# Kernel optimization log

Measured on AMD Instinct MI355X. Metric: run time of the kernel, lower is better.

## Reference

```python
import jax, jax.numpy as jnp
import numpy as np

E, D, H, N = 8, 1024, 4096, 8192  # experts, model dim, moe intermediate, total tokens


def setup_inputs() -> dict:
    key = jax.random.key(0)
    k0, k1, k2, k3 = jax.random.split(key, 4)
    x = jax.random.normal(k0, (N, D), jnp.float32)
    # PrimeRL layout: w1,w3: [E, H, D]; w2: [E, D, H]
    w1 = jax.random.normal(k1, (E, H, D), jnp.float32) * 0.02
    w2 = jax.random.normal(k2, (E, D, H), jnp.float32) * 0.02
    w3 = jax.random.normal(k3, (E, H, D), jnp.float32) * 0.02
    num_tokens_per_expert = jnp.full((E,), N // E, dtype=jnp.int32)  # balanced, sums to N
    return {"x": x, "w1": w1, "w2": w2, "w3": w3,
            "num_tokens_per_expert": num_tokens_per_expert}


def reference(x, w1, w2, w3, num_tokens_per_expert):
    # grouped MoE FFN: per expert e over its contiguous token block,
    #   h = gelu_tanh(x @ w1[e].T) * (x @ w3[e].T); out = h @ w2[e].T
    # torch path casts to bf16 for the grouped mm, casts output back.
    gs = num_tokens_per_expert.astype(jnp.int32)  # group sizes = offsets via cumsum
    xb = x.astype(jnp.bfloat16)
    w1t = jnp.swapaxes(w1, -2, -1).astype(jnp.bfloat16)  # [E, D, H]
    w2t = jnp.swapaxes(w2, -2, -1).astype(jnp.bfloat16)  # [E, H, D]
    w3t = jnp.swapaxes(w3, -2, -1).astype(jnp.bfloat16)  # [E, D, H]
    g = jax.lax.ragged_dot(xb, w1t, gs)                  # [N, H]
    h = jax.nn.gelu(g, approximate=True) * jax.lax.ragged_dot(xb, w3t, gs)
    out = jax.lax.ragged_dot(h, w2t, gs).astype(x.dtype)  # [N, D]
    return out
```

## Files before the change

kernel.cpp:

```cpp
#include <hip/hip_runtime.h>
#include <hip/hip_bf16.h>

#define E_ 8
#define D_ 1024
#define H_ 4096
#define N_ 8192

typedef __attribute__((ext_vector_type(8))) short bf16x8;
typedef __attribute__((ext_vector_type(4))) float f32x4;
typedef unsigned short u16;

static __device__ __forceinline__ u16 f2bf(float f) {
    unsigned int u = __float_as_uint(f);
    u += 0x7fffu + ((u >> 16) & 1u);
    return (u16)(u >> 16);
}

static __device__ __forceinline__ void st_bf4(u16* p, float4 v) {
    union { u16 u[4]; unsigned long long ll; } t;
    t.u[0] = f2bf(v.x); t.u[1] = f2bf(v.y); t.u[2] = f2bf(v.z); t.u[3] = f2bf(v.w);
    *(unsigned long long*)p = t.ll;
}

static __device__ __forceinline__ float gelu_tanh(float x) {
    float x3 = x * x * x;
    float z = 0.7978845608028654f * (x + 0.044715f * x3);
    float t = 1.0f - 2.0f / (1.0f + __expf(2.0f * z));
    return 0.5f * x * (1.0f + t);
}

static __device__ __forceinline__ int expert_of(const int* __restrict__ ntpe, int row) {
    int acc = 0;
    #pragma unroll
    for (int i = 0; i < E_; ++i) {
        acc += ntpe[i];
        if (row < acc) return i;
    }
    return E_ - 1;
}

#define GLD16(gp, lp) __builtin_amdgcn_global_load_lds( \
    (const __attribute__((address_space(1))) void*)(gp), \
    (__attribute__((address_space(3))) void*)(lp), 16, 0, 0)

#define CVT_XBLK 512
#define CVT_WBLK 2048
#define CVT_NBLK (CVT_XBLK + 3 * CVT_WBLK)

__global__ __launch_bounds__(256) void cvt_all2(
    const float* __restrict__ x, const float* __restrict__ w1,
    const float* __restrict__ w2, const float* __restrict__ w3,
    u16* __restrict__ xb, u16* __restrict__ w1b,
    u16* __restrict__ w2b, u16* __restrict__ w3b)
{
    int b = blockIdx.x;
    const float* src; u16* dst; int n8; int b0; int nb;
    if (b < CVT_XBLK) {
        src = x; dst = xb; n8 = N_ * D_ / 8; b0 = 0; nb = CVT_XBLK;
    } else if (b < CVT_XBLK + CVT_WBLK) {
        src = w1; dst = w1b; n8 = E_ * H_ * D_ / 8; b0 = CVT_XBLK; nb = CVT_WBLK;
    } else if (b < CVT_XBLK + 2 * CVT_WBLK) {
        src = w2; dst = w2b; n8 = E_ * D_ * H_ / 8; b0 = CVT_XBLK + CVT_WBLK; nb = CVT_WBLK;
    } else {
        src = w3; dst = w3b; n8 = E_ * H_ * D_ / 8; b0 = CVT_XBLK + 2 * CVT_WBLK; nb = CVT_WBLK;
    }
    int t = (b - b0) * 256 + threadIdx.x;
    int stride = nb * 256;
    const float4* s4 = (const float4*)src;
    for (int i = t; i < n8; i += stride) {
        float4 a = s4[i * 2];
        float4 c = s4[i * 2 + 1];
        union { u16 u[8]; bf16x8 v; } o;
        o.u[0] = f2bf(a.x); o.u[1] = f2bf(a.y); o.u[2] = f2bf(a.z); o.u[3] = f2bf(a.w);
        o.u[4] = f2bf(c.x); o.u[5] = f2bf(c.y); o.u[6] = f2bf(c.z); o.u[7] = f2bf(c.w);
        *(bf16x8*)(dst + (size_t)i * 8) = o.v;
    }
}

#define EPIT 72

__global__ __launch_bounds__(256, 3) void moe_gemm13_fast(
    const u16* __restrict__ xb, const u16* __restrict__ w1b,
    const u16* __restrict__ w3b, const int* __restrict__ ntpe,
    u16* __restrict__ hbuf)
{
    __shared__ u16 smem[128 * EPIT];
    u16* sA  = smem;
    u16* sB1 = smem + 4096;
    u16* sB2 = smem + 6144;

    const int tid = threadIdx.x;
    const int m0 = blockIdx.y * 128, n0 = blockIdx.x * 64;
    const int e = expert_of(ntpe, m0);
    const int wave = tid >> 6, lane = tid & 63;
    const int wm = (wave >> 1) * 64, wn = (wave & 1) * 32;
    const int fr = lane & 15, quad = lane >> 4;

    const u16* Ag  = xb  + (size_t)m0 * D_;
    const u16* B1g = w1b + ((size_t)e * H_ + n0) * D_;
    const u16* B2g = w3b + ((size_t)e * H_ + n0) * D_;

    const int srA = wave * 32 + (lane >> 2);
    const int srB = wave * 16 + (lane >> 2);
    const int scol = (lane & 3) * 8;

    f32x4 accg[4][2], accu[4][2];
    #pragma unroll
    for (int i = 0; i < 4; ++i)
        #pragma unroll
        for (int j = 0; j < 2; ++j) {
            accg[i][j] = (f32x4){0.f, 0.f, 0.f, 0.f};
            accu[i][j] = (f32x4){0.f, 0.f, 0.f, 0.f};
        }

    for (int k0 = 0; k0 < D_; k0 += 32) {
        #pragma unroll
        for (int c = 0; c < 2; ++c)
            GLD16(Ag + (size_t)(srA + c * 16) * D_ + k0 + scol, sA + (wave * 32 + c * 16) * 32);
        GLD16(B1g + (size_t)srB * D_ + k0 + scol, sB1 + wave * 16 * 32);
        GLD16(B2g + (size_t)srB * D_ + k0 + scol, sB2 + wave * 16 * 32);
        __syncthreads();

        bf16x8 fa[4], fb1[2], fb2[2];
        #pragma unroll
        for (int i = 0; i < 4; ++i)
            fa[i] = *(const bf16x8*)(&sA[(wm + i * 16 + fr) * 32 + quad * 8]);
        #pragma unroll
        for (int j = 0; j < 2; ++j) {
            fb1[j] = *(const bf16x8*)(&sB1[(wn + j * 16 + fr) * 32 + quad * 8]);
            fb2[j] = *(const bf16x8*)(&sB2[(wn + j * 16 + fr) * 32 + quad * 8]);
        }
        #pragma unroll
        for (int i = 0; i < 4; ++i)
            #pragma unroll
            for (int j = 0; j < 2; ++j) {
                accg[i][j] = __builtin_amdgcn_mfma_f32_16x16x32_bf16(fa[i], fb1[j], accg[i][j], 0, 0, 0);
                accu[i][j] = __builtin_amdgcn_mfma_f32_16x16x32_bf16(fa[i], fb2[j], accu[i][j], 0, 0, 0);
            }
        __syncthreads();
    }

    #pragma unroll
    for (int i = 0; i < 4; ++i) {
        int rl = wm + i * 16 + quad * 4;
        #pragma unroll
        for (int j = 0; j < 2; ++j) {
            int cl = wn + j * 16 + fr;
            #pragma unroll
            for (int r = 0; r < 4; ++r) {
                float hv = gelu_tanh(accg[i][j][r]) * accu[i][j][r];
                smem[(rl + r) * EPIT + cl] = f2bf(hv);
            }
        }
    }
    __syncthreads();
    #pragma unroll
    for (int it = 0; it < 4; ++it) {
        int chunk = it * 256 + tid;
        int row = chunk >> 3;
        int col = (chunk & 7) * 8;
        bf16x8 v = *(const bf16x8*)(&smem[row * EPIT + col]);
        *(bf16x8*)(&hbuf[(size_t)(m0 + row) * H_ + n0 + col]) = v;
    }
}

__global__ __launch_bounds__(256, 3) void moe_gemm2_fast(
    const u16* __restrict__ hbuf, const u16* __restrict__ w2b,
    const int* __restrict__ ntpe, float* __restrict__ out)
{
    __shared__ u16 sA[128 * 32], sB[128 * 32];
    const int tid = threadIdx.x;
    const int m0 = blockIdx.y * 128, n0 = blockIdx.x * 128;
    const int e = expert_of(ntpe, m0);
    const int wave = tid >> 6, lane = tid & 63;
    const int wm = (wave >> 1) * 64, wn = (wave & 1) * 64;
    const int fr = lane & 15, quad = lane >> 4;

    const u16* Ag = hbuf + (size_t)m0 * H_;
    const u16* Bg = w2b + ((size_t)e * D_ + n0) * H_;

    const int srow = wave * 32 + (lane >> 2);
    const int scol = (lane & 3) * 8;

    f32x4 acc[4][4];
    #pragma unroll
    for (int i = 0; i < 4; ++i)
        #pragma unroll
        for (int j = 0; j < 4; ++j)
            acc[i][j] = (f32x4){0.f, 0.f, 0.f, 0.f};

    for (int k0 = 0; k0 < H_; k0 += 32) {
        #pragma unroll
        for (int c = 0; c < 2; ++c) {
            size_t go = (size_t)(srow + c * 16) * H_ + k0 + scol;
            int lb = (wave * 2 + c) * 16 * 32;
            GLD16(Ag + go, &sA[lb]);
            GLD16(Bg + go, &sB[lb]);
        }
        __syncthreads();

        bf16x8 fa[4], fb[4];
        #pragma unroll
        for (int i = 0; i < 4; ++i) {
            fa[i] = *(const bf16x8*)(&sA[(wm + i * 16 + fr) * 32 + quad * 8]);
            fb[i] = *(const bf16x8*)(&sB[(wn + i * 16 + fr) * 32 + quad * 8]);
        }
        #pragma unroll
        for (int i = 0; i < 4; ++i)
            #pragma unroll
            for (int j = 0; j < 4; ++j)
                acc[i][j] = __builtin_amdgcn_mfma_f32_16x16x32_bf16(fa[i], fb[j], acc[i][j], 0, 0, 0);
        __syncthreads();
    }

    #pragma unroll
    for (int i = 0; i < 4; ++i) {
        int rowb = m0 + wm + i * 16 + quad * 4;
        #pragma unroll
        for (int j = 0; j < 4; ++j) {
            int col = n0 + wn + j * 16 + fr;
            #pragma unroll
            for (int r = 0; r < 4; ++r)
                out[(size_t)(rowb + r) * D_ + col] = acc[i][j][r];
        }
    }
}

#define LDSP 40

__global__ __launch_bounds__(256, 2) void moe_gemm13_slow(
    const float* __restrict__ x, const float* __restrict__ w1,
    const float* __restrict__ w3, const int* __restrict__ ntpe,
    u16* __restrict__ hbuf)
{
    const int tid = threadIdx.x;
    const int m0 = blockIdx.y * 128, n0 = blockIdx.x * 128;
    const int e = expert_of(ntpe, m0);
    __shared__ u16 sA[128][LDSP]; __shared__ u16 sB1[128][LDSP]; __shared__ u16 sB2[128][LDSP];
    const int wave = tid >> 6, lane = tid & 63;
    const int wm = (wave >> 1) * 64, wn = (wave & 1) * 64;
    const int fr = lane & 15, quad = lane >> 4;
    f32x4 accg[4][4], accu[4][4];
    #pragma unroll
    for (int i = 0; i < 4; ++i)
        #pragma unroll
        for (int j = 0; j < 4; ++j) {
            accg[i][j] = (f32x4){0.f,0.f,0.f,0.f}; accu[i][j] = (f32x4){0.f,0.f,0.f,0.f};
        }
    const float* Ab  = x  + (size_t)m0 * D_;
    const float* B1b = w1 + ((size_t)e * H_ + n0) * D_;
    const float* B2b = w3 + ((size_t)e * H_ + n0) * D_;
    for (int k0 = 0; k0 < D_; k0 += 32) {
        #pragma unroll
        for (int s = 0; s < 4; ++s) {
            int idx = s * 256 + tid;
            int row = idx >> 3, col = (idx & 7) * 4;
            size_t go = (size_t)row * D_ + k0 + col;
            st_bf4(&sA[row][col],  *(const float4*)(Ab + go));
            st_bf4(&sB1[row][col], *(const float4*)(B1b + go));
            st_bf4(&sB2[row][col], *(const float4*)(B2b + go));
        }
        __syncthreads();
        bf16x8 fa[4], fb1[4], fb2[4];
        #pragma unroll
        for (int i = 0; i < 4; ++i) {
            fa[i]  = *(const bf16x8*)(&sA[wm + i * 16 + fr][quad * 8]);
            fb1[i] = *(const bf16x8*)(&sB1[wn + i * 16 + fr][quad * 8]);
            fb2[i] = *(const bf16x8*)(&sB2[wn + i * 16 + fr][quad * 8]);
        }
        #pragma unroll
        for (int i = 0; i < 4; ++i)
            #pragma unroll
            for (int j = 0; j < 4; ++j) {
                accg[i][j] = __builtin_amdgcn_mfma_f32_16x16x32_bf16(fa[i], fb1[j], accg[i][j], 0, 0, 0);
                accu[i][j] = __builtin_amdgcn_mfma_f32_16x16x32_bf16(fa[i], fb2[j], accu[i][j], 0, 0, 0);
            }
        __syncthreads();
    }
    #pragma unroll
    for (int i = 0; i < 4; ++i) {
        int rowb = m0 + wm + i * 16 + quad * 4;
        #pragma unroll
        for (int j = 0; j < 4; ++j) {
            int col = n0 + wn + j * 16 + fr;
            #pragma unroll
            for (int r = 0; r < 4; ++r)
                hbuf[(size_t)(rowb + r) * H_ + col] = f2bf(gelu_tanh(accg[i][j][r]) * accu[i][j][r]);
        }
    }
}

__global__ __launch_bounds__(256, 2) void moe_gemm2_slow(
    const u16* __restrict__ hbuf, const float* __restrict__ w2,
    const int* __restrict__ ntpe, float* __restrict__ out)
{
    const int tid = threadIdx.x;
    const int m0 = blockIdx.y * 128, n0 = blockIdx.x * 128;
    const int e = expert_of(ntpe, m0);
    __shared__ u16 sA[128][LDSP]; __shared__ u16 sB[128][LDSP];
    const int wave = tid >> 6, lane = tid & 63;
    const int wm = (wave >> 1) * 64, wn = (wave & 1) * 64;
    const int fr = lane & 15, quad = lane >> 4;
    f32x4 acc[4][4];
    #pragma unroll
    for (int i = 0; i < 4; ++i)
        #pragma unroll
        for (int j = 0; j < 4; ++j) acc[i][j] = (f32x4){0.f,0.f,0.f,0.f};
    const u16* Ab = hbuf + (size_t)m0 * H_;
    const float* Bb = w2 + ((size_t)e * D_ + n0) * H_;
    for (int k0 = 0; k0 < H_; k0 += 32) {
        #pragma unroll
        for (int s = 0; s < 2; ++s) {
            int idx = s * 256 + tid;
            int row = idx >> 2, col = (idx & 3) * 8;
            *(bf16x8*)(&sA[row][col]) = *(const bf16x8*)(Ab + (size_t)row * H_ + k0 + col);
        }
        #pragma unroll
        for (int s = 0; s < 4; ++s) {
            int idx = s * 256 + tid;
            int row = idx >> 3, col = (idx & 7) * 4;
            st_bf4(&sB[row][col], *(const float4*)(Bb + (size_t)row * H_ + k0 + col));
        }
        __syncthreads();
        bf16x8 fa[4], fb[4];
        #pragma unroll
        for (int i = 0; i < 4; ++i) {
            fa[i] = *(const bf16x8*)(&sA[wm + i * 16 + fr][quad * 8]);
            fb[i] = *(const bf16x8*)(&sB[wn + i * 16 + fr][quad * 8]);
        }
        #pragma unroll
        for (int i = 0; i < 4; ++i)
            #pragma unroll
            for (int j = 0; j < 4; ++j)
                acc[i][j] = __builtin_amdgcn_mfma_f32_16x16x32_bf16(fa[i], fb[j], acc[i][j], 0, 0, 0);
        __syncthreads();
    }
    #pragma unroll
    for (int i = 0; i < 4; ++i) {
        int rowb = m0 + wm + i * 16 + quad * 4;
        #pragma unroll
        for (int j = 0; j < 4; ++j) {
            int col = n0 + wn + j * 16 + fr;
            #pragma unroll
            for (int r = 0; r < 4; ++r)
                out[(size_t)(rowb + r) * D_ + col] = acc[i][j][r];
        }
    }
}

extern "C" void kernel_launch(void* const* d_in, const int* in_sizes, int n_in,
                              void* d_out, int out_size, void* d_ws, size_t ws_size,
                              hipStream_t stream) {
    const float* x  = (const float*)d_in[0];
    const float* w1 = (const float*)d_in[1];
    const float* w2 = (const float*)d_in[2];
    const float* w3 = (const float*)d_in[3];
    const int* ntpe = (const int*)d_in[4];
    float* out = (float*)d_out;

    const size_t SZ_XB = (size_t)N_ * D_ * 2;
    const size_t SZ_W  = (size_t)E_ * H_ * D_ * 2;
    const size_t SZ_H  = (size_t)N_ * H_ * 2;
    const size_t NEED  = SZ_XB + 3 * SZ_W + SZ_H;

    if (ws_size >= NEED) {
        char* p = (char*)d_ws;
        u16* xb  = (u16*)p;                 p += SZ_XB;
        u16* w1b = (u16*)p;                 p += SZ_W;
        u16* w3b = (u16*)p;                 p += SZ_W;
        u16* w2b = (u16*)p;                 p += SZ_W;
        u16* hb  = (u16*)p;

        cvt_all2<<<CVT_NBLK, 256, 0, stream>>>(x, w1, w2, w3, xb, w1b, w2b, w3b);

        dim3 g1(H_ / 64, N_ / 128);
        moe_gemm13_fast<<<g1, 256, 0, stream>>>(xb, w1b, w3b, ntpe, hb);

        dim3 g2(D_ / 128, N_ / 128);
        moe_gemm2_fast<<<g2, 256, 0, stream>>>(hb, w2b, ntpe, out);
    } else {
        u16* hb = (u16*)d_ws;
        dim3 g1(H_ / 128, N_ / 128);
        moe_gemm13_slow<<<g1, 256, 0, stream>>>(x, w1, w3, ntpe, hb);
        dim3 g2(D_ / 128, N_ / 128);
        moe_gemm2_slow<<<g2, 256, 0, stream>>>(hb, w2, ntpe, out);
    }
}
```

Measured before the change: 705.5 us.

## Double K-step to 64 and XOR-swizzle LDS layout in both MoE GEMMs

Both GEMM kernels now stage a 64-wide K slice per iteration instead of 32. This halves the number of barrier pairs per tile and doubles the MFMA work between syncs. Global-to-LDS loads use a row-dependent XOR swizzle on the 16-byte column groups, with matching swizzled fragment reads, to avoid LDS bank conflicts on the 128-byte row stride. LDS use per block doubles to 32 KB, which may limit how many blocks fit per CU alongside the launch-bounds target of 3.

```diff
diff --git a/kernel.cpp b/kernel.cpp
--- a/kernel.cpp
+++ b/kernel.cpp
@@ -77,6 +77,7 @@
     }
 }
 
+
 #define EPIT 72
 
 __global__ __launch_bounds__(256, 3) void moe_gemm13_fast(
@@ -84,10 +85,10 @@
     const u16* __restrict__ w3b, const int* __restrict__ ntpe,
     u16* __restrict__ hbuf)
 {
-    __shared__ u16 smem[128 * EPIT];
+    __shared__ u16 smem[16384];
     u16* sA  = smem;
-    u16* sB1 = smem + 4096;
-    u16* sB2 = smem + 6144;
+    u16* sB1 = smem + 8192;
+    u16* sB2 = smem + 12288;
 
     const int tid = threadIdx.x;
     const int m0 = blockIdx.y * 128, n0 = blockIdx.x * 64;
@@ -95,14 +96,14 @@
     const int wave = tid >> 6, lane = tid & 63;
     const int wm = (wave >> 1) * 64, wn = (wave & 1) * 32;
     const int fr = lane & 15, quad = lane >> 4;
+    const int sw = fr & 7;
 
     const u16* Ag  = xb  + (size_t)m0 * D_;
     const u16* B1g = w1b + ((size_t)e * H_ + n0) * D_;
     const u16* B2g = w3b + ((size_t)e * H_ + n0) * D_;
 
-    const int srA = wave * 32 + (lane >> 2);
-    const int srB = wave * 16 + (lane >> 2);
-    const int scol = (lane & 3) * 8;
+    const int srr = lane >> 3;
+    const int scg = ((lane & 7) ^ srr) * 8;
 
     f32x4 accg[4][2], accu[4][2];
     #pragma unroll
@@ -113,30 +114,40 @@
             accu[i][j] = (f32x4){0.f, 0.f, 0.f, 0.f};
         }
 
-    for (int k0 = 0; k0 < D_; k0 += 32) {
-        #pragma unroll
-        for (int c = 0; c < 2; ++c)
-            GLD16(Ag + (size_t)(srA + c * 16) * D_ + k0 + scol, sA + (wave * 32 + c * 16) * 32);
-        GLD16(B1g + (size_t)srB * D_ + k0 + scol, sB1 + wave * 16 * 32);
-        GLD16(B2g + (size_t)srB * D_ + k0 + scol, sB2 + wave * 16 * 32);
-        __syncthreads();
-
-        bf16x8 fa[4], fb1[2], fb2[2];
-        #pragma unroll
-        for (int i = 0; i < 4; ++i)
-            fa[i] = *(const bf16x8*)(&sA[(wm + i * 16 + fr) * 32 + quad * 8]);
-        #pragma unroll
-        for (int j = 0; j < 2; ++j) {
-            fb1[j] = *(const bf16x8*)(&sB1[(wn + j * 16 + fr) * 32 + quad * 8]);
-            fb2[j] = *(const bf16x8*)(&sB2[(wn + j * 16 + fr) * 32 + quad * 8]);
-        }
-        #pragma unroll
-        for (int i = 0; i < 4; ++i)
+    for (int k0 = 0; k0 < D_; k0 += 64) {
+        #pragma unroll
+        for (int c = 0; c < 4; ++c)
+            GLD16(Ag + (size_t)(wave * 32 + c * 8 + srr) * D_ + k0 + scg,
+                  sA + (wave * 32 + c * 8) * 64);
+        #pragma unroll
+        for (int c = 0; c < 2; ++c) {
+            GLD16(B1g + (size_t)(wave * 16 + c * 8 + srr) * D_ + k0 + scg,
+                  sB1 + (wave * 16 + c * 8) * 64);
+            GLD16(B2g + (size_t)(wave * 16 + c * 8 + srr) * D_ + k0 + scg,
+                  sB2 + (wave * 16 + c * 8) * 64);
+        }
+        __syncthreads();
+
+        #pragma unroll
+        for (int kh = 0; kh < 2; ++kh) {
+            const int ks = ((quad + kh * 4) ^ sw) * 8;
+            bf16x8 fa[4], fb1[2], fb2[2];
+            #pragma unroll
+            for (int i = 0; i < 4; ++i)
+                fa[i] = *(const bf16x8*)(&sA[(wm + i * 16 + fr) * 64 + ks]);
             #pragma unroll
             for (int j = 0; j < 2; ++j) {
-                accg[i][j] = __builtin_amdgcn_mfma_f32_16x16x32_bf16(fa[i], fb1[j], accg[i][j], 0, 0, 0);
-                accu[i][j] = __builtin_amdgcn_mfma_f32_16x16x32_bf16(fa[i], fb2[j], accu[i][j], 0, 0, 0);
+                fb1[j] = *(const bf16x8*)(&sB1[(wn + j * 16 + fr) * 64 + ks]);
+                fb2[j] = *(const bf16x8*)(&sB2[(wn + j * 16 + fr) * 64 + ks]);
             }
+            #pragma unroll
+            for (int i = 0; i < 4; ++i)
+                #pragma unroll
+                for (int j = 0; j < 2; ++j) {
+                    accg[i][j] = __builtin_amdgcn_mfma_f32_16x16x32_bf16(fa[i], fb1[j], accg[i][j], 0, 0, 0);
+                    accu[i][j] = __builtin_amdgcn_mfma_f32_16x16x32_bf16(fa[i], fb2[j], accu[i][j], 0, 0, 0);
+                }
+        }
         __syncthreads();
     }
 
@@ -168,19 +179,23 @@
     const u16* __restrict__ hbuf, const u16* __restrict__ w2b,
     const int* __restrict__ ntpe, float* __restrict__ out)
 {
-    __shared__ u16 sA[128 * 32], sB[128 * 32];
+    __shared__ u16 smem[16384];
+    u16* sA = smem;
+    u16* sB = smem + 8192;
+
     const int tid = threadIdx.x;
     const int m0 = blockIdx.y * 128, n0 = blockIdx.x * 128;
     const int e = expert_of(ntpe, m0);
     const int wave = tid >> 6, lane = tid & 63;
     const int wm = (wave >> 1) * 64, wn = (wave & 1) * 64;
     const int fr = lane & 15, quad = lane >> 4;
+    const int sw = fr & 7;
 
     const u16* Ag = hbuf + (size_t)m0 * H_;
     const u16* Bg = w2b + ((size_t)e * D_ + n0) * H_;
 
-    const int srow = wave * 32 + (lane >> 2);
-    const int scol = (lane & 3) * 8;
+    const int srr = lane >> 3;
+    const int scg = ((lane & 7) ^ srr) * 8;
 
     f32x4 acc[4][4];
     #pragma unroll
@@ -189,27 +204,31 @@
         for (int j = 0; j < 4; ++j)
             acc[i][j] = (f32x4){0.f, 0.f, 0.f, 0.f};
 
-    for (int k0 = 0; k0 < H_; k0 += 32) {
-        #pragma unroll
-        for (int c = 0; c < 2; ++c) {
-            size_t go = (size_t)(srow + c * 16) * H_ + k0 + scol;
-            int lb = (wave * 2 + c) * 16 * 32;
-            GLD16(Ag + go, &sA[lb]);
-            GLD16(Bg + go, &sB[lb]);
-        }
-        __syncthreads();
-
-        bf16x8 fa[4], fb[4];
-        #pragma unroll
-        for (int i = 0; i < 4; ++i) {
-            fa[i] = *(const bf16x8*)(&sA[(wm + i * 16 + fr) * 32 + quad * 8]);
-            fb[i] = *(const bf16x8*)(&sB[(wn + i * 16 + fr) * 32 + quad * 8]);
-        }
-        #pragma unroll
-        for (int i = 0; i < 4; ++i)
-            #pragma unroll
-            for (int j = 0; j < 4; ++j)
-                acc[i][j] = __builtin_amdgcn_mfma_f32_16x16x32_bf16(fa[i], fb[j], acc[i][j], 0, 0, 0);
+    for (int k0 = 0; k0 < H_; k0 += 64) {
+        #pragma unroll
+        for (int c = 0; c < 4; ++c) {
+            GLD16(Ag + (size_t)(wave * 32 + c * 8 + srr) * H_ + k0 + scg,
+                  sA + (wave * 32 + c * 8) * 64);
+            GLD16(Bg + (size_t)(wave * 32 + c * 8 + srr) * H_ + k0 + scg,
+                  sB + (wave * 32 + c * 8) * 64);
+        }
+        __syncthreads();
+
+        #pragma unroll
+        for (int kh = 0; kh < 2; ++kh) {
+            const int ks = ((quad + kh * 4) ^ sw) * 8;
+            bf16x8 fa[4], fb[4];
+            #pragma unroll
+            for (int i = 0; i < 4; ++i) {
+                fa[i] = *(const bf16x8*)(&sA[(wm + i * 16 + fr) * 64 + ks]);
+                fb[i] = *(const bf16x8*)(&sB[(wn + i * 16 + fr) * 64 + ks]);
+            }
+            #pragma unroll
+            for (int i = 0; i < 4; ++i)
+                #pragma unroll
+                for (int j = 0; j < 4; ++j)
+                    acc[i][j] = __builtin_amdgcn_mfma_f32_16x16x32_bf16(fa[i], fb[j], acc[i][j], 0, 0, 0);
+        }
         __syncthreads();
     }
 
```

After: 644.5 us. 8.6% less time.
